# Kernel optimization log

Measured on AMD Instinct MI355X. Metric: run time of the kernel, lower is better.

Reference implementation:

```python
import jax, jax.numpy as jnp
import numpy as np

HEADS = 8
MODEL_DIM = 64
EPS = 1e-5


def _layernorm(x, gamma, beta):
    mu = jnp.mean(x, axis=-1, keepdims=True)
    var = jnp.var(x, axis=-1, keepdims=True)
    return (x - mu) * jax.lax.rsqrt(var + EPS) * gamma + beta


def setup_inputs() -> dict:
    key = jax.random.key(0)
    ks = jax.random.split(key, 5)
    bs, h, w, in_dim = 8, 32, 32, 512
    hd = HEADS * MODEL_DIM  # 512
    s = 0.02
    return {
        "x": jax.random.normal(ks[0], (bs, h, w, in_dim), jnp.float32),
        "Wq": jax.random.normal(ks[1], (in_dim, hd), jnp.float32) * s,
        "Wk": jax.random.normal(ks[2], (in_dim, hd), jnp.float32) * s,
        "Wv": jax.random.normal(ks[3], (in_dim, hd), jnp.float32) * s,
        "Wo": jax.random.normal(ks[4], (hd, in_dim), jnp.float32) * s,
        "gamma": jnp.ones((in_dim,), jnp.float32),
        "beta": jnp.zeros((in_dim,), jnp.float32),
    }


def reference(x, Wq, Wk, Wv, Wo, gamma, beta):
    bs, h, w, in_dim = x.shape
    # pre_norm=True: normalize first; residual uses the normalized x (as in original)
    xn = _layernorm(x, gamma, beta)
    Q = (xn @ Wq).reshape(bs, h, w, HEADS, MODEL_DIM)
    K = (xn @ Wk).reshape(bs, h, w, HEADS, MODEL_DIM)
    V = (xn @ Wv).reshape(bs, h, w, HEADS, MODEL_DIM)
    # full (h,w) x (h,w) correlation per head
    corr = jnp.einsum('bijhd,bklhd->bijhkl', Q, K) / jnp.sqrt(
        jnp.asarray(MODEL_DIM, x.dtype))
    cshape = corr.shape
    attn = jax.nn.softmax(corr.reshape(*cshape[:-2], -1), axis=-1).reshape(cshape)
    logits = jnp.einsum('bijhkl,bklhd->bijhd', attn, V).reshape(bs, h, w, -1)
    out = logits @ Wo + xn
    return out, attn
```

## Files before the change

### kernel.cpp

```cpp
#include <hip/hip_runtime.h>
#include <hip/hip_bf16.h>

typedef __attribute__((ext_vector_type(8))) short bf16x8;
typedef __attribute__((ext_vector_type(4))) short s16x4;
typedef __attribute__((ext_vector_type(4))) float f32x4;

#define DIM 512
#define NH 8
#define HD 64
#define SEQ 1024
#define NB 8
#define ROWS (NB*SEQ)

__device__ __forceinline__ short f2bf(float f) {
  union { float f; unsigned u; } v; v.f = f;
  unsigned r = v.u + 0x7fffu + ((v.u >> 16) & 1u);
  return (short)(r >> 16);
}
__device__ __forceinline__ float bf2f(short s) {
  union { unsigned u; float f; } v; v.u = ((unsigned)(unsigned short)s) << 16;
  return v.f;
}
__device__ __forceinline__ f32x4 mfma16(bf16x8 a, bf16x8 b, f32x4 c) {
  return __builtin_amdgcn_mfma_f32_16x16x32_bf16(a, b, c, 0, 0, 0);
}
__device__ __forceinline__ void gload16(const void* g, void* l) {
  __builtin_amdgcn_global_load_lds(
      (const __attribute__((address_space(1))) unsigned int*)g,
      (__attribute__((address_space(3))) unsigned int*)l, 16, 0, 0);
}
__device__ __forceinline__ void lds_barrier() {
  __builtin_amdgcn_sched_barrier(0);
  asm volatile("s_waitcnt lgkmcnt(0)" ::: "memory");
  __builtin_amdgcn_s_barrier();
  __builtin_amdgcn_sched_barrier(0);
}

__global__ __launch_bounds__(256) void ln_kernel(const float* __restrict__ x,
    const float* __restrict__ gamma, const float* __restrict__ beta,
    short* __restrict__ xnb) {
  const int t = threadIdx.x;
  const int row = blockIdx.x * 4 + (t >> 6);
  const int lane = t & 63;
  const float4* xr = reinterpret_cast<const float4*>(x + (size_t)row * DIM);
  const float4 a = xr[lane * 2], b2 = xr[lane * 2 + 1];
  float s = a.x + a.y + a.z + a.w + b2.x + b2.y + b2.z + b2.w;
  float sq = a.x*a.x + a.y*a.y + a.z*a.z + a.w*a.w +
             b2.x*b2.x + b2.y*b2.y + b2.z*b2.z + b2.w*b2.w;
  for (int off = 1; off < 64; off <<= 1) {
    s += __shfl_xor(s, off);
    sq += __shfl_xor(sq, off);
  }
  const float mean = s * (1.0f / DIM);
  const float var = sq * (1.0f / DIM) - mean * mean;
  const float rs = rsqrtf(var + 1e-5f);
  const float4 ga = reinterpret_cast<const float4*>(gamma)[lane * 2];
  const float4 gb = reinterpret_cast<const float4*>(gamma)[lane * 2 + 1];
  const float4 ba = reinterpret_cast<const float4*>(beta)[lane * 2];
  const float4 bb = reinterpret_cast<const float4*>(beta)[lane * 2 + 1];
  union { bf16x8 v; short sh[8]; } o;
  o.sh[0] = f2bf((a.x - mean) * rs * ga.x + ba.x);
  o.sh[1] = f2bf((a.y - mean) * rs * ga.y + ba.y);
  o.sh[2] = f2bf((a.z - mean) * rs * ga.z + ba.z);
  o.sh[3] = f2bf((a.w - mean) * rs * ga.w + ba.w);
  o.sh[4] = f2bf((b2.x - mean) * rs * gb.x + bb.x);
  o.sh[5] = f2bf((b2.y - mean) * rs * gb.y + bb.y);
  o.sh[6] = f2bf((b2.z - mean) * rs * gb.z + bb.z);
  o.sh[7] = f2bf((b2.w - mean) * rs * gb.w + bb.w);
  *reinterpret_cast<bf16x8*>(xnb + (size_t)row * DIM + lane * 8) = o.v;
}

__global__ __launch_bounds__(256) void wtrans_kernel(
    const float* __restrict__ Wq, const float* __restrict__ Wk,
    const float* __restrict__ Wv, const float* __restrict__ Wo,
    short* __restrict__ WqkvT, short* __restrict__ WoT) {
  __shared__ float tl[64 * 65];
  const int y = blockIdx.y;
  const float* W = (y == 0) ? Wq : (y == 1) ? Wk : (y == 2) ? Wv : Wo;
  const int tile = blockIdx.x;
  const int k0 = (tile >> 3) * 64, n0 = (tile & 7) * 64;
  const int t = threadIdx.x;
#pragma unroll
  for (int i = 0; i < 16; ++i) {
    const int idx = i * 256 + t;
    const int k = idx >> 6, n = idx & 63;
    tl[n * 65 + k] = W[(size_t)(k0 + k) * 512 + n0 + n];
  }
  __syncthreads();
#pragma unroll
  for (int i = 0; i < 16; ++i) {
    const int idx = i * 256 + t;
    const int n = idx >> 6, k = idx & 63;
    const short v = f2bf(tl[n * 65 + k]);
    if (y < 3) WqkvT[(size_t)(y * 512 + n0 + n) * 512 + k0 + k] = v;
    else       WoT[(size_t)(n0 + n) * 512 + k0 + k] = v;
  }
}

#define GEMM64_MAIN(A_, BT_, m0_, n0_)                                        \
  f32x4 acc[4][4] = {};                                                       \
  {                                                                           \
    const int srow = 8 * w + (lane >> 3);                                     \
    const int sseg = lane & 7;                                                \
    for (int kb = 0; kb < 512; kb += 64) {                                    \
      __syncthreads();                                                        \
      _Pragma("unroll")                                                       \
      for (int p = 0; p < 4; ++p) {                                           \
        const int r = 32 * p + srow;                                          \
        const int gs = 8 * (sseg ^ (r & 7));                                  \
        gload16(A_ + (size_t)(m0_ + r) * 512 + kb + gs,                       \
                &As[(32 * p + 8 * w) * 64]);                                  \
        gload16(BT_ + (size_t)(n0_ + r) * 512 + kb + gs,                      \
                &Bs[(32 * p + 8 * w) * 64]);                                  \
      }                                                                       \
      __syncthreads();                                                        \
      _Pragma("unroll")                                                       \
      for (int half = 0; half < 2; ++half) {                                  \
        bf16x8 af[4], bfr[4];                                                 \
        _Pragma("unroll")                                                     \
        for (int i = 0; i < 4; ++i) {                                         \
          const int ra = 64 * wr + 16 * i + c16;                              \
          af[i] = *reinterpret_cast<const bf16x8*>(                           \
              &As[ra * 64 + 8 * ((4 * half + g) ^ (ra & 7))]);                \
          const int rb = 64 * wc + 16 * i + c16;                              \
          bfr[i] = *reinterpret_cast<const bf16x8*>(                          \
              &Bs[rb * 64 + 8 * ((4 * half + g) ^ (rb & 7))]);                \
        }                                                                     \
        _Pragma("unroll")                                                     \
        for (int i = 0; i < 4; ++i)                                           \
          _Pragma("unroll")                                                   \
          for (int j = 0; j < 4; ++j)                                         \
            acc[i][j] = mfma16(af[i], bfr[j], acc[i][j]);                     \
      }                                                                       \
    }                                                                         \
  }

__global__ __launch_bounds__(256) void gemm_qkv(const short* __restrict__ A,
    const short* __restrict__ BT, short* __restrict__ Qo,
    short* __restrict__ Ko, short* __restrict__ VtF) {
  __shared__ short As[128 * 64];
  __shared__ short Bs[128 * 64];
  const int m0 = blockIdx.x * 128, n0 = blockIdx.y * 128;
  const int t = threadIdx.x, w = t >> 6, lane = t & 63, g = lane >> 4, c16 = lane & 15;
  const int wr = w >> 1, wc = w & 1;
  GEMM64_MAIN(A, BT, m0, n0)
  const int z = n0 >> 9;
  const int nl = n0 & 511;
#pragma unroll
  for (int i = 0; i < 4; ++i)
#pragma unroll
    for (int j = 0; j < 4; ++j)
#pragma unroll
      for (int e = 0; e < 4; ++e) {
        const int row = m0 + 64 * wr + 16 * i + 4 * g + e;
        const int col = nl + 64 * wc + 16 * j + c16;
        const short v = f2bf(acc[i][j][e]);
        if (z == 0) {
          Qo[(size_t)row * 512 + col] = v;
        } else if (z == 1) {
          Ko[(size_t)row * 512 + col] = v;
        } else {
          const int bb = row >> 10, ss = row & 1023, hh = col >> 6, dd = col & 63;
          const int cch = ss >> 7, kk = ss & 127;
          const int w2 = kk >> 5, g2 = (kk >> 3) & 3, ee = kk & 7;
          const int dt2 = dd >> 4, c162 = dd & 15;
          VtF[((size_t)((((bb * NH + hh) * 8 + cch) * 4 + w2) * 4 + dt2) << 9) +
              (g2 * 16 + c162) * 8 + ee] = v;
        }
      }
}

__global__ __launch_bounds__(256) void gemm_out(const short* __restrict__ A,
    const short* __restrict__ BT, const short* __restrict__ xnb,
    float* __restrict__ out) {
  __shared__ short As[128 * 64];
  __shared__ short Bs[128 * 64];
  const int m0 = blockIdx.x * 128, n0 = blockIdx.y * 128;
  const int t = threadIdx.x, w = t >> 6, lane = t & 63, g = lane >> 4, c16 = lane & 15;
  const int wr = w >> 1, wc = w & 1;
  GEMM64_MAIN(A, BT, m0, n0)
#pragma unroll
  for (int i = 0; i < 4; ++i)
#pragma unroll
    for (int j = 0; j < 4; ++j)
#pragma unroll
      for (int e = 0; e < 4; ++e) {
        const int row = m0 + 64 * wr + 16 * i + 4 * g + e;
        const int col = n0 + 64 * wc + 16 * j + c16;
        const size_t idx = (size_t)row * 512 + col;
        out[idx] = acc[i][j][e] + bf2f(xnb[idx]);
      }
}

__global__ __launch_bounds__(256) void attn_kernel(
    const short* __restrict__ Qb, const short* __restrict__ Kb,
    const short* __restrict__ VtF, float* __restrict__ attnOut,
    short* __restrict__ Lg) {
  const int bid = blockIdx.x;
  const int rb = (bid >> 3) & 63;
  const int inst = (bid & 7) * 8 + (bid >> 9);
  const int b = inst >> 3, h = inst & 7;
  const int t = threadIdx.x;
  const int w = t >> 6, lane = t & 63, g = lane >> 4, c16 = lane & 15;
  const int rl = lane >> 3, sgl = lane & 7;

  __shared__ __align__(16) char smem[32768];
  __shared__ float red[2][4][16];
  short* Klds = (short*)smem;
  float* P32a = (float*)smem;
  float* P32b = (float*)(smem + 8448);
  short* P16 = (short*)(smem + 16896);

  const short* qp = Qb + ((size_t)(b * SEQ + rb * 16 + c16)) * DIM + h * HD + 8 * g;
  const bf16x8 qf0 = *reinterpret_cast<const bf16x8*>(qp);
  const bf16x8 qf1 = *reinterpret_cast<const bf16x8*>(qp + 32);

  const short* kgbase = Kb + ((size_t)b * SEQ) * DIM + h * HD;
  const int swz = 8 * (sgl ^ rl);

#define KSTAGE(c_, buf_)                                                       \
  do {                                                                         \
    __builtin_amdgcn_sched_barrier(0);                                         \
    _Pragma("unroll") for (int i_ = 0; i_ < 4; ++i_) {                         \
      gload16(kgbase + (size_t)((c_) * 128 + 32 * w + 8 * i_ + rl) * DIM + swz,\
              &Klds[(buf_) * 8192 + (32 * w + 8 * i_) * 64]);                  \
    }                                                                          \
  } while (0)

  KSTAGE(0, 0);
  f32x4 acc[16] = {};
  const int sw = c16 & 7;
#pragma unroll
  for (int c = 0; c < 8; ++c) {
    if (c < 7) KSTAGE(c + 1, (c + 1) & 1);
    if (c < 7) { asm volatile("s_waitcnt vmcnt(4)" ::: "memory"); }
    else       { asm volatile("s_waitcnt vmcnt(0)" ::: "memory"); }
    __builtin_amdgcn_sched_barrier(0);
    const short* kl = &Klds[(c & 1) * 8192];
#pragma unroll
    for (int j = 0; j < 2; ++j) {
      const int lr = 32 * w + 16 * j + c16;
      bf16x8 k0 = *reinterpret_cast<const bf16x8*>(&kl[lr * 64 + 8 * (g ^ sw)]);
      bf16x8 k1 = *reinterpret_cast<const bf16x8*>(&kl[lr * 64 + 8 * ((g + 4) ^ sw)]);
      const int tt = c * 2 + j;
      acc[tt] = mfma16(k0, qf0, acc[tt]);
      acc[tt] = mfma16(k1, qf1, acc[tt]);
    }
  }

  const short* vf = VtF + (size_t)inst * 65536;
  bf16x8 vreg[4];
#pragma unroll
  for (int dt = 0; dt < 4; ++dt)
    vreg[dt] = *reinterpret_cast<const bf16x8*>(vf + (size_t)((w * 4 + dt) * 512) + lane * 8);

  float m = -1e30f;
#pragma unroll
  for (int tt = 0; tt < 16; ++tt)
#pragma unroll
    for (int e = 0; e < 4; ++e) {
      acc[tt][e] *= 0.125f;
      m = fmaxf(m, acc[tt][e]);
    }
  m = fmaxf(m, __shfl_xor(m, 16));
  m = fmaxf(m, __shfl_xor(m, 32));
  if (g == 0) red[0][w][c16] = m;
  lds_barrier();
  m = fmaxf(fmaxf(red[0][0][c16], red[0][1][c16]),
            fmaxf(red[0][2][c16], red[0][3][c16]));
  float sm = 0.f;
#pragma unroll
  for (int tt = 0; tt < 16; ++tt)
#pragma unroll
    for (int e = 0; e < 4; ++e) {
      const float p = __expf(acc[tt][e] - m);
      acc[tt][e] = p;
      sm += p;
    }
  sm += __shfl_xor(sm, 16);
  sm += __shfl_xor(sm, 32);
  if (g == 0) red[1][w][c16] = sm;
  lds_barrier();
  const float rinv = 1.0f / (red[1][0][c16] + red[1][1][c16] +
                             red[1][2][c16] + red[1][3][c16]);

  f32x4 pacc[4] = {};
  const int qrow = t >> 4, qs = t & 15;
  float* abase2 = attnOut + (size_t)b * 8388608 +
                  (size_t)(rb * 16 + qrow) * 8192 + h * 1024;
#pragma unroll
  for (int c = 0; c < 8; ++c) {
    float* P32w = (c & 1) ? P32b : P32a;
#pragma unroll
    for (int j = 0; j < 2; ++j) {
      const int col = 32 * w + 16 * j + 4 * g;
      f32x4 pv;
#pragma unroll
      for (int e = 0; e < 4; ++e) pv[e] = acc[2 * c + j][e] * rinv;
      *reinterpret_cast<f32x4*>(&P32w[c16 * 132 + col]) = pv;
      s16x4 pb;
#pragma unroll
      for (int e = 0; e < 4; ++e) pb[e] = f2bf(pv[e]);
      *reinterpret_cast<s16x4*>(&P16[c16 * 136 + col]) = pb;
    }
    {
      const bf16x8 pa = *reinterpret_cast<const bf16x8*>(
          &P16[c16 * 136 + 32 * w + 8 * g]);
#pragma unroll
      for (int dt = 0; dt < 4; ++dt)
        pacc[dt] = mfma16(pa, vreg[dt], pacc[dt]);
    }
    if (c < 7) {
#pragma unroll
      for (int dt = 0; dt < 4; ++dt)
        vreg[dt] = *reinterpret_cast<const bf16x8*>(
            vf + (size_t)((((c + 1) * 4 + w) * 4 + dt) * 512) + lane * 8);
    }
    lds_barrier();
    {
      float* arow = abase2 + c * 128;
      const float* P32r = (c & 1) ? P32b : P32a;
      const f32x4 s0 = *reinterpret_cast<const f32x4*>(&P32r[qrow * 132 + 4 * qs]);
      const f32x4 s1 = *reinterpret_cast<const f32x4*>(&P32r[qrow * 132 + 64 + 4 * qs]);
      __builtin_nontemporal_store(s0, reinterpret_cast<f32x4*>(arow + 4 * qs));
      __builtin_nontemporal_store(s1, reinterpret_cast<f32x4*>(arow + 64 + 4 * qs));
    }
  }

  lds_barrier();
  f32x4* red2 = reinterpret_cast<f32x4*>(smem);
#pragma unroll
  for (int dt = 0; dt < 4; ++dt) red2[(w * 4 + dt) * 64 + lane] = pacc[dt];
  lds_barrier();
  {
    const int dt = w;
    f32x4 s = red2[dt * 64 + lane];
#pragma unroll
    for (int w2 = 1; w2 < 4; ++w2) {
      f32x4 o = red2[(w2 * 4 + dt) * 64 + lane];
#pragma unroll
      for (int e = 0; e < 4; ++e) s[e] += o[e];
    }
    short* lrow = Lg + ((size_t)(b * SEQ + rb * 16 + 4 * g)) * DIM + h * HD + 16 * dt + c16;
#pragma unroll
    for (int e = 0; e < 4; ++e) lrow[(size_t)e * DIM] = f2bf(s[e]);
  }
}

extern "C" void kernel_launch(void* const* d_in, const int* in_sizes, int n_in,
                              void* d_out, int out_size, void* d_ws, size_t ws_size,
                              hipStream_t stream) {
  const float* x = (const float*)d_in[0];
  const float* Wq = (const float*)d_in[1];
  const float* Wk = (const float*)d_in[2];
  const float* Wv = (const float*)d_in[3];
  const float* Wo = (const float*)d_in[4];
  const float* gamma = (const float*)d_in[5];
  const float* beta = (const float*)d_in[6];
  float* out = (float*)d_out;
  float* attn = out + (size_t)ROWS * DIM;

  char* ws = (char*)d_ws;
  short* xnb = (short*)ws;
  short* WqkvT = (short*)(ws + (size_t)8 * 1024 * 1024);
  short* WoT = WqkvT + 1536 * 512;
  short* Qb = (short*)(ws + (size_t)10 * 1024 * 1024);
  short* Kbp = (short*)(ws + (size_t)18 * 1024 * 1024);
  short* VtF = (short*)(ws + (size_t)26 * 1024 * 1024);
  short* Lg = (short*)(ws + (size_t)34 * 1024 * 1024);

  ln_kernel<<<2048, 256, 0, stream>>>(x, gamma, beta, xnb);
  wtrans_kernel<<<dim3(64, 4), 256, 0, stream>>>(Wq, Wk, Wv, Wo, WqkvT, WoT);
  gemm_qkv<<<dim3(64, 12), 256, 0, stream>>>(xnb, WqkvT, Qb, Kbp, VtF);
  attn_kernel<<<4096, 256, 0, stream>>>(Qb, Kbp, VtF, attn, Lg);
  gemm_out<<<dim3(64, 4), 256, 0, stream>>>(Lg, WoT, xnb, out);
}
```

Before: 139.5 us.

## Process two query row-blocks per attention block, overlapping second QK with first output

Each attention workgroup now handles 32 query rows (two 16-row halves) instead of 16, halving the grid. While the first half's attention probabilities are written out and multiplied with V, the second half's QK^T is computed using K tiles prefetched through registers into LDS, so the K loads and MFMAs overlap the large attention-matrix stores. The attention values written out are now rounded through bf16 before being stored as fp32, which slightly changes output precision. LDS use grows and launch bounds request 2 blocks per CU, which raises register pressure.

After: 128.3 us. -8.1%, faster.

```diff
diff --git a/kernel.cpp b/kernel.cpp
--- a/kernel.cpp
+++ b/kernel.cpp
@@ -192,31 +192,33 @@
       }
 }
 
-__global__ __launch_bounds__(256) void attn_kernel(
+__global__ __launch_bounds__(256, 2) void attn_kernel(
     const short* __restrict__ Qb, const short* __restrict__ Kb,
     const short* __restrict__ VtF, float* __restrict__ attnOut,
     short* __restrict__ Lg) {
   const int bid = blockIdx.x;
-  const int rb = (bid >> 3) & 63;
-  const int inst = (bid & 7) * 8 + (bid >> 9);
+  const int rb = (bid >> 3) & 31;
+  const int inst = (bid & 7) * 8 + (bid >> 8);
   const int b = inst >> 3, h = inst & 7;
   const int t = threadIdx.x;
   const int w = t >> 6, lane = t & 63, g = lane >> 4, c16 = lane & 15;
   const int rl = lane >> 3, sgl = lane & 7;
 
-  __shared__ __align__(16) char smem[32768];
+  __shared__ __align__(16) char smem[49664];
   __shared__ float red[2][4][16];
   short* Klds = (short*)smem;
-  float* P32a = (float*)smem;
-  float* P32b = (float*)(smem + 8448);
-  short* P16 = (short*)(smem + 16896);
-
-  const short* qp = Qb + ((size_t)(b * SEQ + rb * 16 + c16)) * DIM + h * HD + 8 * g;
-  const bf16x8 qf0 = *reinterpret_cast<const bf16x8*>(qp);
-  const bf16x8 qf1 = *reinterpret_cast<const bf16x8*>(qp + 32);
+  float* P32a = (float*)(smem + 32768);
+  float* P32b = (float*)(smem + 41216);
+
+  const short* qpa = Qb + ((size_t)(b * SEQ + rb * 32 + c16)) * DIM + h * HD + 8 * g;
+  const bf16x8 qa0 = *reinterpret_cast<const bf16x8*>(qpa);
+  const bf16x8 qa1 = *reinterpret_cast<const bf16x8*>(qpa + 32);
+  const bf16x8 qB0 = *reinterpret_cast<const bf16x8*>(qpa + 16 * DIM);
+  const bf16x8 qB1 = *reinterpret_cast<const bf16x8*>(qpa + 16 * DIM + 32);
 
   const short* kgbase = Kb + ((size_t)b * SEQ) * DIM + h * HD;
   const int swz = 8 * (sgl ^ rl);
+  const int sw = c16 & 7;
 
 #define KSTAGE(c_, buf_)                                                       \
   do {                                                                         \
@@ -229,7 +231,6 @@
 
   KSTAGE(0, 0);
   f32x4 acc[16] = {};
-  const int sw = c16 & 7;
 #pragma unroll
   for (int c = 0; c < 8; ++c) {
     if (c < 7) KSTAGE(c + 1, (c + 1) & 1);
@@ -243,8 +244,8 @@
       bf16x8 k0 = *reinterpret_cast<const bf16x8*>(&kl[lr * 64 + 8 * (g ^ sw)]);
       bf16x8 k1 = *reinterpret_cast<const bf16x8*>(&kl[lr * 64 + 8 * ((g + 4) ^ sw)]);
       const int tt = c * 2 + j;
-      acc[tt] = mfma16(k0, qf0, acc[tt]);
-      acc[tt] = mfma16(k1, qf1, acc[tt]);
+      acc[tt] = mfma16(k0, qa0, acc[tt]);
+      acc[tt] = mfma16(k1, qa1, acc[tt]);
     }
   }
 
@@ -253,6 +254,11 @@
 #pragma unroll
   for (int dt = 0; dt < 4; ++dt)
     vreg[dt] = *reinterpret_cast<const bf16x8*>(vf + (size_t)((w * 4 + dt) * 512) + lane * 8);
+  bf16x8 kreg[4];
+#pragma unroll
+  for (int i = 0; i < 4; ++i)
+    kreg[i] = *reinterpret_cast<const bf16x8*>(
+        kgbase + (size_t)(32 * w + 8 * i + rl) * DIM + 8 * sgl);
 
   float m = -1e30f;
 #pragma unroll
@@ -281,56 +287,162 @@
   sm += __shfl_xor(sm, 32);
   if (g == 0) red[1][w][c16] = sm;
   lds_barrier();
-  const float rinv = 1.0f / (red[1][0][c16] + red[1][1][c16] +
-                             red[1][2][c16] + red[1][3][c16]);
-
-  f32x4 pacc[4] = {};
+  const float rinvA = 1.0f / (red[1][0][c16] + red[1][1][c16] +
+                              red[1][2][c16] + red[1][3][c16]);
+
+  bf16x8 pA[8];
+#pragma unroll
+  for (int c = 0; c < 8; ++c) {
+    union { bf16x8 v; short sh[8]; } u;
+#pragma unroll
+    for (int j = 0; j < 2; ++j)
+#pragma unroll
+      for (int e = 0; e < 4; ++e)
+        u.sh[4 * j + e] = f2bf(acc[2 * c + j][e] * rinvA);
+    pA[c] = u.v;
+  }
+#pragma unroll
+  for (int tt = 0; tt < 16; ++tt)
+#pragma unroll
+    for (int e = 0; e < 4; ++e) acc[tt][e] = 0.f;
+
+  f32x4 paccA[4] = {};
   const int qrow = t >> 4, qs = t & 15;
-  float* abase2 = attnOut + (size_t)b * 8388608 +
-                  (size_t)(rb * 16 + qrow) * 8192 + h * 1024;
+  float* astore = attnOut + (size_t)b * 8388608 +
+                  (size_t)(rb * 32 + qrow) * 8192 + h * 1024;
 #pragma unroll
   for (int c = 0; c < 8; ++c) {
-    float* P32w = (c & 1) ? P32b : P32a;
+    lds_barrier();
+#pragma unroll
+    for (int i = 0; i < 4; ++i)
+      *reinterpret_cast<bf16x8*>(
+          &Klds[(c & 1) * 8192 + (32 * w + 8 * i + rl) * 64 + 8 * (sgl ^ rl)]) = kreg[i];
+    {
+      float* P32w = (c & 1) ? P32b : P32a;
+      union { bf16x8 v; short sh[8]; } u; u.v = pA[c];
+      f32x4 v0, v1;
+#pragma unroll
+      for (int e = 0; e < 4; ++e) { v0[e] = bf2f(u.sh[e]); v1[e] = bf2f(u.sh[4 + e]); }
+      *reinterpret_cast<f32x4*>(&P32w[c16 * 132 + 32 * w + 4 * g]) = v0;
+      *reinterpret_cast<f32x4*>(&P32w[c16 * 132 + 32 * w + 16 + 4 * g]) = v1;
+    }
+    if (c < 7) {
+#pragma unroll
+      for (int i = 0; i < 4; ++i)
+        kreg[i] = *reinterpret_cast<const bf16x8*>(
+            kgbase + (size_t)((c + 1) * 128 + 32 * w + 8 * i + rl) * DIM + 8 * sgl);
+    }
+    lds_barrier();
+    {
+      const float* P32r = (c & 1) ? P32b : P32a;
+      const f32x4 s0 = *reinterpret_cast<const f32x4*>(&P32r[qrow * 132 + 4 * qs]);
+      const f32x4 s1 = *reinterpret_cast<const f32x4*>(&P32r[qrow * 132 + 64 + 4 * qs]);
+      __builtin_nontemporal_store(s0, reinterpret_cast<f32x4*>(astore + c * 128 + 4 * qs));
+      __builtin_nontemporal_store(s1, reinterpret_cast<f32x4*>(astore + c * 128 + 64 + 4 * qs));
+    }
+    const short* kl = &Klds[(c & 1) * 8192];
 #pragma unroll
     for (int j = 0; j < 2; ++j) {
-      const int col = 32 * w + 16 * j + 4 * g;
-      f32x4 pv;
-#pragma unroll
-      for (int e = 0; e < 4; ++e) pv[e] = acc[2 * c + j][e] * rinv;
-      *reinterpret_cast<f32x4*>(&P32w[c16 * 132 + col]) = pv;
-      s16x4 pb;
-#pragma unroll
-      for (int e = 0; e < 4; ++e) pb[e] = f2bf(pv[e]);
-      *reinterpret_cast<s16x4*>(&P16[c16 * 136 + col]) = pb;
-    }
-    {
-      const bf16x8 pa = *reinterpret_cast<const bf16x8*>(
-          &P16[c16 * 136 + 32 * w + 8 * g]);
-#pragma unroll
-      for (int dt = 0; dt < 4; ++dt)
-        pacc[dt] = mfma16(pa, vreg[dt], pacc[dt]);
-    }
+      const int lr = 32 * w + 16 * j + c16;
+      bf16x8 k0 = *reinterpret_cast<const bf16x8*>(&kl[lr * 64 + 8 * (g ^ sw)]);
+      bf16x8 k1 = *reinterpret_cast<const bf16x8*>(&kl[lr * 64 + 8 * ((g + 4) ^ sw)]);
+      const int tt = c * 2 + j;
+      acc[tt] = mfma16(k0, qB0, acc[tt]);
+      acc[tt] = mfma16(k1, qB1, acc[tt]);
+    }
+#pragma unroll
+    for (int dt = 0; dt < 4; ++dt)
+      paccA[dt] = mfma16(pA[c], vreg[dt], paccA[dt]);
     if (c < 7) {
 #pragma unroll
       for (int dt = 0; dt < 4; ++dt)
         vreg[dt] = *reinterpret_cast<const bf16x8*>(
             vf + (size_t)((((c + 1) * 4 + w) * 4 + dt) * 512) + lane * 8);
     }
+  }
+
+#pragma unroll
+  for (int dt = 0; dt < 4; ++dt)
+    vreg[dt] = *reinterpret_cast<const bf16x8*>(vf + (size_t)((w * 4 + dt) * 512) + lane * 8);
+
+  float mB = -1e30f;
+#pragma unroll
+  for (int tt = 0; tt < 16; ++tt)
+#pragma unroll
+    for (int e = 0; e < 4; ++e) {
+      acc[tt][e] *= 0.125f;
+      mB = fmaxf(mB, acc[tt][e]);
+    }
+  mB = fmaxf(mB, __shfl_xor(mB, 16));
+  mB = fmaxf(mB, __shfl_xor(mB, 32));
+  if (g == 0) red[0][w][c16] = mB;
+  lds_barrier();
+  mB = fmaxf(fmaxf(red[0][0][c16], red[0][1][c16]),
+             fmaxf(red[0][2][c16], red[0][3][c16]));
+  float smB = 0.f;
+#pragma unroll
+  for (int tt = 0; tt < 16; ++tt)
+#pragma unroll
+    for (int e = 0; e < 4; ++e) {
+      const float p = __expf(acc[tt][e] - mB);
+      acc[tt][e] = p;
+      smB += p;
+    }
+  smB += __shfl_xor(smB, 16);
+  smB += __shfl_xor(smB, 32);
+  if (g == 0) red[1][w][c16] = smB;
+  lds_barrier();
+  const float rinvB = 1.0f / (red[1][0][c16] + red[1][1][c16] +
+                              red[1][2][c16] + red[1][3][c16]);
+  bf16x8 pB[8];
+#pragma unroll
+  for (int c = 0; c < 8; ++c) {
+    union { bf16x8 v; short sh[8]; } u;
+#pragma unroll
+    for (int j = 0; j < 2; ++j)
+#pragma unroll
+      for (int e = 0; e < 4; ++e)
+        u.sh[4 * j + e] = f2bf(acc[2 * c + j][e] * rinvB);
+    pB[c] = u.v;
+  }
+
+  f32x4 paccB[4] = {};
+  float* astoreB = astore + 16 * 8192;
+#pragma unroll
+  for (int c = 0; c < 8; ++c) {
     lds_barrier();
     {
-      float* arow = abase2 + c * 128;
+      float* P32w = (c & 1) ? P32b : P32a;
+      union { bf16x8 v; short sh[8]; } u; u.v = pB[c];
+      f32x4 v0, v1;
+#pragma unroll
+      for (int e = 0; e < 4; ++e) { v0[e] = bf2f(u.sh[e]); v1[e] = bf2f(u.sh[4 + e]); }
+      *reinterpret_cast<f32x4*>(&P32w[c16 * 132 + 32 * w + 4 * g]) = v0;
+      *reinterpret_cast<f32x4*>(&P32w[c16 * 132 + 32 * w + 16 + 4 * g]) = v1;
+    }
+    lds_barrier();
+    {
       const float* P32r = (c & 1) ? P32b : P32a;
       const f32x4 s0 = *reinterpret_cast<const f32x4*>(&P32r[qrow * 132 + 4 * qs]);
       const f32x4 s1 = *reinterpret_cast<const f32x4*>(&P32r[qrow * 132 + 64 + 4 * qs]);
-      __builtin_nontemporal_store(s0, reinterpret_cast<f32x4*>(arow + 4 * qs));
-      __builtin_nontemporal_store(s1, reinterpret_cast<f32x4*>(arow + 64 + 4 * qs));
+      __builtin_nontemporal_store(s0, reinterpret_cast<f32x4*>(astoreB + c * 128 + 4 * qs));
+      __builtin_nontemporal_store(s1, reinterpret_cast<f32x4*>(astoreB + c * 128 + 64 + 4 * qs));
+    }
+#pragma unroll
+    for (int dt = 0; dt < 4; ++dt)
+      paccB[dt] = mfma16(pB[c], vreg[dt], paccB[dt]);
+    if (c < 7) {
+#pragma unroll
+      for (int dt = 0; dt < 4; ++dt)
+        vreg[dt] = *reinterpret_cast<const bf16x8*>(
+            vf + (size_t)((((c + 1) * 4 + w) * 4 + dt) * 512) + lane * 8);
     }
   }
 
   lds_barrier();
   f32x4* red2 = reinterpret_cast<f32x4*>(smem);
 #pragma unroll
-  for (int dt = 0; dt < 4; ++dt) red2[(w * 4 + dt) * 64 + lane] = pacc[dt];
+  for (int dt = 0; dt < 4; ++dt) red2[(w * 4 + dt) * 64 + lane] = paccA[dt];
   lds_barrier();
   {
     const int dt = w;
@@ -341,7 +453,24 @@
 #pragma unroll
       for (int e = 0; e < 4; ++e) s[e] += o[e];
     }
-    short* lrow = Lg + ((size_t)(b * SEQ + rb * 16 + 4 * g)) * DIM + h * HD + 16 * dt + c16;
+    short* lrow = Lg + ((size_t)(b * SEQ + rb * 32 + 4 * g)) * DIM + h * HD + 16 * dt + c16;
+#pragma unroll
+    for (int e = 0; e < 4; ++e) lrow[(size_t)e * DIM] = f2bf(s[e]);
+  }
+  lds_barrier();
+#pragma unroll
+  for (int dt = 0; dt < 4; ++dt) red2[(w * 4 + dt) * 64 + lane] = paccB[dt];
+  lds_barrier();
+  {
+    const int dt = w;
+    f32x4 s = red2[dt * 64 + lane];
+#pragma unroll
+    for (int w2 = 1; w2 < 4; ++w2) {
+      f32x4 o = red2[(w2 * 4 + dt) * 64 + lane];
+#pragma unroll
+      for (int e = 0; e < 4; ++e) s[e] += o[e];
+    }
+    short* lrow = Lg + ((size_t)(b * SEQ + rb * 32 + 16 + 4 * g)) * DIM + h * HD + 16 * dt + c16;
 #pragma unroll
     for (int e = 0; e < 4; ++e) lrow[(size_t)e * DIM] = f2bf(s[e]);
   }
@@ -372,6 +501,6 @@
   ln_kernel<<<2048, 256, 0, stream>>>(x, gamma, beta, xnb);
   wtrans_kernel<<<dim3(64, 4), 256, 0, stream>>>(Wq, Wk, Wv, Wo, WqkvT, WoT);
   gemm_qkv<<<dim3(64, 12), 256, 0, stream>>>(xnb, WqkvT, Qb, Kbp, VtF);
-  attn_kernel<<<4096, 256, 0, stream>>>(Qb, Kbp, VtF, attn, Lg);
+  attn_kernel<<<2048, 256, 0, stream>>>(Qb, Kbp, VtF, attn, Lg);
   gemm_out<<<dim3(64, 4), 256, 0, stream>>>(Lg, WoT, xnb, out);
 }
```

## Process four query tiles per attention block with software-pipelined QK and PV

Applied to the files above, without the earlier changes.

Each attention block now handles 64 query rows (four 16-row tiles) instead of 16, with a 5-stage loop that overlaps the QK^T of the next tile with the PV product and attn-matrix store of the previous tile. K loading switches from async global-to-LDS loads to register-staged prefetch, and P is kept in bf16 registers and expanded back to fp32 for the attn output. The goal is to amortise per-block setup, hide load latency and keep MFMA busy during the large attention-matrix writes, at the cost of more registers and LDS and a quarter as many blocks. The attn output is now written from bf16-rounded probabilities rather than fp32, which reduces accuracy of the returned attention.

New measurement: 369.9 us. +165.2%, slower.

```diff
diff --git a/kernel.cpp b/kernel.cpp
--- a/kernel.cpp
+++ b/kernel.cpp
@@ -192,158 +192,212 @@
       }
 }
 
-__global__ __launch_bounds__(256) void attn_kernel(
+__global__ __launch_bounds__(256, 2) void attn_kernel(
     const short* __restrict__ Qb, const short* __restrict__ Kb,
     const short* __restrict__ VtF, float* __restrict__ attnOut,
     short* __restrict__ Lg) {
   const int bid = blockIdx.x;
-  const int rb = (bid >> 3) & 63;
-  const int inst = (bid & 7) * 8 + (bid >> 9);
+  const int rb = (bid >> 3) & 15;
+  const int inst = (bid & 7) * 8 + (bid >> 7);
   const int b = inst >> 3, h = inst & 7;
   const int t = threadIdx.x;
   const int w = t >> 6, lane = t & 63, g = lane >> 4, c16 = lane & 15;
   const int rl = lane >> 3, sgl = lane & 7;
-
-  __shared__ __align__(16) char smem[32768];
+  const int sw = c16 & 7;
+  const int rbase = rb * 64;
+
+  __shared__ __align__(16) char smem[49664];
   __shared__ float red[2][4][16];
   short* Klds = (short*)smem;
-  float* P32a = (float*)smem;
-  float* P32b = (float*)(smem + 8448);
-  short* P16 = (short*)(smem + 16896);
-
-  const short* qp = Qb + ((size_t)(b * SEQ + rb * 16 + c16)) * DIM + h * HD + 8 * g;
-  const bf16x8 qf0 = *reinterpret_cast<const bf16x8*>(qp);
-  const bf16x8 qf1 = *reinterpret_cast<const bf16x8*>(qp + 32);
+  float* P32a = (float*)(smem + 32768);
+  float* P32b = (float*)(smem + 41216);
 
   const short* kgbase = Kb + ((size_t)b * SEQ) * DIM + h * HD;
-  const int swz = 8 * (sgl ^ rl);
-
-#define KSTAGE(c_, buf_)                                                       \
-  do {                                                                         \
-    __builtin_amdgcn_sched_barrier(0);                                         \
-    _Pragma("unroll") for (int i_ = 0; i_ < 4; ++i_) {                         \
-      gload16(kgbase + (size_t)((c_) * 128 + 32 * w + 8 * i_ + rl) * DIM + swz,\
-              &Klds[(buf_) * 8192 + (32 * w + 8 * i_) * 64]);                  \
-    }                                                                          \
-  } while (0)
-
-  KSTAGE(0, 0);
+  const short* vf = VtF + (size_t)inst * 65536;
+
+  bf16x8 kreg[4], vreg[4];
+#pragma unroll
+  for (int i = 0; i < 4; ++i)
+    kreg[i] = *reinterpret_cast<const bf16x8*>(
+        kgbase + (size_t)(32 * w + 8 * i + rl) * DIM + 8 * sgl);
+#pragma unroll
+  for (int i = 0; i < 4; ++i)
+    *reinterpret_cast<bf16x8*>(
+        &Klds[(32 * w + 8 * i + rl) * 64 + 8 * (sgl ^ rl)]) = kreg[i];
+#pragma unroll
+  for (int i = 0; i < 4; ++i)
+    kreg[i] = *reinterpret_cast<const bf16x8*>(
+        kgbase + (size_t)(128 + 32 * w + 8 * i + rl) * DIM + 8 * sgl);
+#pragma unroll
+  for (int dt = 0; dt < 4; ++dt)
+    vreg[dt] = *reinterpret_cast<const bf16x8*>(
+        vf + (size_t)((w * 4 + dt) * 512) + lane * 8);
+
+  const short* q0p = Qb + ((size_t)(b * SEQ + rbase + c16)) * DIM + h * HD + 8 * g;
+  bf16x8 q0 = *reinterpret_cast<const bf16x8*>(q0p);
+  bf16x8 q1 = *reinterpret_cast<const bf16x8*>(q0p + 32);
+
   f32x4 acc[16] = {};
-  const int sw = c16 & 7;
-#pragma unroll
-  for (int c = 0; c < 8; ++c) {
-    if (c < 7) KSTAGE(c + 1, (c + 1) & 1);
-    if (c < 7) { asm volatile("s_waitcnt vmcnt(4)" ::: "memory"); }
-    else       { asm volatile("s_waitcnt vmcnt(0)" ::: "memory"); }
-    __builtin_amdgcn_sched_barrier(0);
-    const short* kl = &Klds[(c & 1) * 8192];
-#pragma unroll
-    for (int j = 0; j < 2; ++j) {
-      const int lr = 32 * w + 16 * j + c16;
-      bf16x8 k0 = *reinterpret_cast<const bf16x8*>(&kl[lr * 64 + 8 * (g ^ sw)]);
-      bf16x8 k1 = *reinterpret_cast<const bf16x8*>(&kl[lr * 64 + 8 * ((g + 4) ^ sw)]);
-      const int tt = c * 2 + j;
-      acc[tt] = mfma16(k0, qf0, acc[tt]);
-      acc[tt] = mfma16(k1, qf1, acc[tt]);
-    }
-  }
-
-  const short* vf = VtF + (size_t)inst * 65536;
-  bf16x8 vreg[4];
-#pragma unroll
-  for (int dt = 0; dt < 4; ++dt)
-    vreg[dt] = *reinterpret_cast<const bf16x8*>(vf + (size_t)((w * 4 + dt) * 512) + lane * 8);
-
-  float m = -1e30f;
-#pragma unroll
-  for (int tt = 0; tt < 16; ++tt)
-#pragma unroll
-    for (int e = 0; e < 4; ++e) {
-      acc[tt][e] *= 0.125f;
-      m = fmaxf(m, acc[tt][e]);
-    }
-  m = fmaxf(m, __shfl_xor(m, 16));
-  m = fmaxf(m, __shfl_xor(m, 32));
-  if (g == 0) red[0][w][c16] = m;
-  lds_barrier();
-  m = fmaxf(fmaxf(red[0][0][c16], red[0][1][c16]),
-            fmaxf(red[0][2][c16], red[0][3][c16]));
-  float sm = 0.f;
-#pragma unroll
-  for (int tt = 0; tt < 16; ++tt)
-#pragma unroll
-    for (int e = 0; e < 4; ++e) {
-      const float p = __expf(acc[tt][e] - m);
-      acc[tt][e] = p;
-      sm += p;
-    }
-  sm += __shfl_xor(sm, 16);
-  sm += __shfl_xor(sm, 32);
-  if (g == 0) red[1][w][c16] = sm;
-  lds_barrier();
-  const float rinv = 1.0f / (red[1][0][c16] + red[1][1][c16] +
-                             red[1][2][c16] + red[1][3][c16]);
-
-  f32x4 pacc[4] = {};
+  bf16x8 pA[8];
+  f32x4 pacc[4] = {{0.f,0.f,0.f,0.f},{0.f,0.f,0.f,0.f},{0.f,0.f,0.f,0.f},{0.f,0.f,0.f,0.f}};
+
   const int qrow = t >> 4, qs = t & 15;
-  float* abase2 = attnOut + (size_t)b * 8388608 +
-                  (size_t)(rb * 16 + qrow) * 8192 + h * 1024;
-#pragma unroll
-  for (int c = 0; c < 8; ++c) {
-    float* P32w = (c & 1) ? P32b : P32a;
-#pragma unroll
-    for (int j = 0; j < 2; ++j) {
-      const int col = 32 * w + 16 * j + 4 * g;
-      f32x4 pv;
-#pragma unroll
-      for (int e = 0; e < 4; ++e) pv[e] = acc[2 * c + j][e] * rinv;
-      *reinterpret_cast<f32x4*>(&P32w[c16 * 132 + col]) = pv;
-      s16x4 pb;
-#pragma unroll
-      for (int e = 0; e < 4; ++e) pb[e] = f2bf(pv[e]);
-      *reinterpret_cast<s16x4*>(&P16[c16 * 136 + col]) = pb;
-    }
-    {
-      const bf16x8 pa = *reinterpret_cast<const bf16x8*>(
-          &P16[c16 * 136 + 32 * w + 8 * g]);
-#pragma unroll
-      for (int dt = 0; dt < 4; ++dt)
-        pacc[dt] = mfma16(pa, vreg[dt], pacc[dt]);
-    }
-    if (c < 7) {
+  float* ainst = attnOut + (size_t)b * 8388608 + (size_t)h * 1024;
+
+  for (int p = 0; p < 5; ++p) {
+    const bool doQK = (p < 4);
+    const bool doPV = (p >= 1);
+    float* astore = ainst + (size_t)(rbase + (doPV ? (p - 1) : 0) * 16 + qrow) * 8192;
+
+#pragma unroll
+    for (int c = 0; c < 8; ++c) {
+      lds_barrier();
+      if (doQK) {
+#pragma unroll
+        for (int i = 0; i < 4; ++i)
+          *reinterpret_cast<bf16x8*>(
+              &Klds[((c + 1) & 1) * 8192 + (32 * w + 8 * i + rl) * 64 + 8 * (sgl ^ rl)]) = kreg[i];
+      }
+      if (doPV) {
+        float* P32w = (c & 1) ? P32b : P32a;
+        union { bf16x8 v; short sh[8]; } u; u.v = pA[c];
+        f32x4 v0, v1;
+#pragma unroll
+        for (int e = 0; e < 4; ++e) { v0[e] = bf2f(u.sh[e]); v1[e] = bf2f(u.sh[4 + e]); }
+        *reinterpret_cast<f32x4*>(&P32w[c16 * 132 + 32 * w + 4 * g]) = v0;
+        *reinterpret_cast<f32x4*>(&P32w[c16 * 132 + 32 * w + 16 + 4 * g]) = v1;
+      }
+      if (doPV && c >= 1) {
+        const float* P32r = ((c - 1) & 1) ? P32b : P32a;
+        const f32x4 s0 = *reinterpret_cast<const f32x4*>(&P32r[qrow * 132 + 4 * qs]);
+        const f32x4 s1 = *reinterpret_cast<const f32x4*>(&P32r[qrow * 132 + 64 + 4 * qs]);
+        __builtin_nontemporal_store(s0, reinterpret_cast<f32x4*>(astore + (c - 1) * 128 + 4 * qs));
+        __builtin_nontemporal_store(s1, reinterpret_cast<f32x4*>(astore + (c - 1) * 128 + 64 + 4 * qs));
+      }
+      if (doQK) {
+        const short* kl = &Klds[(c & 1) * 8192];
+#pragma unroll
+        for (int j = 0; j < 2; ++j) {
+          const int lr = 32 * w + 16 * j + c16;
+          bf16x8 k0 = *reinterpret_cast<const bf16x8*>(&kl[lr * 64 + 8 * (g ^ sw)]);
+          bf16x8 k1 = *reinterpret_cast<const bf16x8*>(&kl[lr * 64 + 8 * ((g + 4) ^ sw)]);
+          acc[c * 2 + j] = mfma16(k0, q0, acc[c * 2 + j]);
+          acc[c * 2 + j] = mfma16(k1, q1, acc[c * 2 + j]);
+        }
+      }
+      if (doPV) {
+#pragma unroll
+        for (int dt = 0; dt < 4; ++dt)
+          pacc[dt] = mfma16(pA[c], vreg[dt], pacc[dt]);
+      }
+      if (doQK) {
+#pragma unroll
+        for (int i = 0; i < 4; ++i)
+          kreg[i] = *reinterpret_cast<const bf16x8*>(
+              kgbase + (size_t)(((c + 2) & 7) * 128 + 32 * w + 8 * i + rl) * DIM + 8 * sgl);
+      }
 #pragma unroll
       for (int dt = 0; dt < 4; ++dt)
         vreg[dt] = *reinterpret_cast<const bf16x8*>(
-            vf + (size_t)((((c + 1) * 4 + w) * 4 + dt) * 512) + lane * 8);
+            vf + (size_t)(((((c + 1) & 7) * 4 + w) * 4 + dt) * 512) + lane * 8);
     }
-    lds_barrier();
-    {
-      float* arow = abase2 + c * 128;
-      const float* P32r = (c & 1) ? P32b : P32a;
-      const f32x4 s0 = *reinterpret_cast<const f32x4*>(&P32r[qrow * 132 + 4 * qs]);
-      const f32x4 s1 = *reinterpret_cast<const f32x4*>(&P32r[qrow * 132 + 64 + 4 * qs]);
-      __builtin_nontemporal_store(s0, reinterpret_cast<f32x4*>(arow + 4 * qs));
-      __builtin_nontemporal_store(s1, reinterpret_cast<f32x4*>(arow + 64 + 4 * qs));
+
+    if (doPV) {
+      lds_barrier();
+      const f32x4 s0 = *reinterpret_cast<const f32x4*>(&P32b[qrow * 132 + 4 * qs]);
+      const f32x4 s1 = *reinterpret_cast<const f32x4*>(&P32b[qrow * 132 + 64 + 4 * qs]);
+      __builtin_nontemporal_store(s0, reinterpret_cast<f32x4*>(astore + 7 * 128 + 4 * qs));
+      __builtin_nontemporal_store(s1, reinterpret_cast<f32x4*>(astore + 7 * 128 + 64 + 4 * qs));
     }
-  }
-
-  lds_barrier();
-  f32x4* red2 = reinterpret_cast<f32x4*>(smem);
-#pragma unroll
-  for (int dt = 0; dt < 4; ++dt) red2[(w * 4 + dt) * 64 + lane] = pacc[dt];
-  lds_barrier();
-  {
-    const int dt = w;
-    f32x4 s = red2[dt * 64 + lane];
-#pragma unroll
-    for (int w2 = 1; w2 < 4; ++w2) {
-      f32x4 o = red2[(w2 * 4 + dt) * 64 + lane];
-#pragma unroll
-      for (int e = 0; e < 4; ++e) s[e] += o[e];
+    f32x4* red2 = reinterpret_cast<f32x4*>(smem + 32768);
+    if (doQK) {
+      float m = -1e30f;
+#pragma unroll
+      for (int tt = 0; tt < 16; ++tt)
+#pragma unroll
+        for (int e = 0; e < 4; ++e) {
+          acc[tt][e] *= 0.125f;
+          m = fmaxf(m, acc[tt][e]);
+        }
+      m = fmaxf(m, __shfl_xor(m, 16));
+      m = fmaxf(m, __shfl_xor(m, 32));
+      if (g == 0) red[0][w][c16] = m;
+      lds_barrier();
+      if (doPV) {
+#pragma unroll
+        for (int dt = 0; dt < 4; ++dt) red2[(w * 4 + dt) * 64 + lane] = pacc[dt];
+#pragma unroll
+        for (int dt = 0; dt < 4; ++dt)
+#pragma unroll
+          for (int e = 0; e < 4; ++e) pacc[dt][e] = 0.f;
+      }
+      m = fmaxf(fmaxf(red[0][0][c16], red[0][1][c16]),
+                fmaxf(red[0][2][c16], red[0][3][c16]));
+      float sm = 0.f;
+#pragma unroll
+      for (int tt = 0; tt < 16; ++tt)
+#pragma unroll
+        for (int e = 0; e < 4; ++e) {
+          const float pe = __expf(acc[tt][e] - m);
+          acc[tt][e] = pe;
+          sm += pe;
+        }
+      sm += __shfl_xor(sm, 16);
+      sm += __shfl_xor(sm, 32);
+      if (g == 0) red[1][w][c16] = sm;
+      lds_barrier();
+      if (doPV) {
+        const int dt = w;
+        f32x4 s = red2[dt * 64 + lane];
+#pragma unroll
+        for (int w2 = 1; w2 < 4; ++w2) {
+          f32x4 o = red2[(w2 * 4 + dt) * 64 + lane];
+#pragma unroll
+          for (int e = 0; e < 4; ++e) s[e] += o[e];
+        }
+        short* lrow = Lg + ((size_t)(b * SEQ + rbase + (p - 1) * 16 + 4 * g)) * DIM +
+                      h * HD + 16 * dt + c16;
+#pragma unroll
+        for (int e = 0; e < 4; ++e) lrow[(size_t)e * DIM] = f2bf(s[e]);
+      }
+      const float rinv = 1.0f / (red[1][0][c16] + red[1][1][c16] +
+                                 red[1][2][c16] + red[1][3][c16]);
+#pragma unroll
+      for (int c = 0; c < 8; ++c) {
+        union { bf16x8 v; short sh[8]; } u;
+#pragma unroll
+        for (int j = 0; j < 2; ++j)
+#pragma unroll
+          for (int e = 0; e < 4; ++e) {
+            u.sh[4 * j + e] = f2bf(acc[2 * c + j][e] * rinv);
+            acc[2 * c + j][e] = 0.f;
+          }
+        pA[c] = u.v;
+      }
+      if (p < 3) {
+        const short* qn = Qb + ((size_t)(b * SEQ + rbase + (p + 1) * 16 + c16)) * DIM +
+                          h * HD + 8 * g;
+        q0 = *reinterpret_cast<const bf16x8*>(qn);
+        q1 = *reinterpret_cast<const bf16x8*>(qn + 32);
+      }
+    } else {
+      lds_barrier();
+#pragma unroll
+      for (int dt = 0; dt < 4; ++dt) red2[(w * 4 + dt) * 64 + lane] = pacc[dt];
+      lds_barrier();
+      const int dt = w;
+      f32x4 s = red2[dt * 64 + lane];
+#pragma unroll
+      for (int w2 = 1; w2 < 4; ++w2) {
+        f32x4 o = red2[(w2 * 4 + dt) * 64 + lane];
+#pragma unroll
+        for (int e = 0; e < 4; ++e) s[e] += o[e];
+      }
+      short* lrow = Lg + ((size_t)(b * SEQ + rbase + 48 + 4 * g)) * DIM +
+                    h * HD + 16 * dt + c16;
+#pragma unroll
+      for (int e = 0; e < 4; ++e) lrow[(size_t)e * DIM] = f2bf(s[e]);
     }
-    short* lrow = Lg + ((size_t)(b * SEQ + rb * 16 + 4 * g)) * DIM + h * HD + 16 * dt + c16;
-#pragma unroll
-    for (int e = 0; e < 4; ++e) lrow[(size_t)e * DIM] = f2bf(s[e]);
   }
 }
 
@@ -372,6 +426,6 @@
   ln_kernel<<<2048, 256, 0, stream>>>(x, gamma, beta, xnb);
   wtrans_kernel<<<dim3(64, 4), 256, 0, stream>>>(Wq, Wk, Wv, Wo, WqkvT, WoT);
   gemm_qkv<<<dim3(64, 12), 256, 0, stream>>>(xnb, WqkvT, Qb, Kbp, VtF);
-  attn_kernel<<<4096, 256, 0, stream>>>(Qb, Kbp, VtF, attn, Lg);
+  attn_kernel<<<1024, 256, 0, stream>>>(Qb, Kbp, VtF, attn, Lg);
   gemm_out<<<dim3(64, 4), 256, 0, stream>>>(Lg, WoT, xnb, out);
 }
```
